# Performance work log

Hardware: AMD Instinct MI355X
Metric: run time of the kernel (lower is better)

## Reference

```python
import jax, jax.numpy as jnp
import numpy as np

PATCH = 128
FEATHER = 4  # config.fusion_feather_size
EPS = 1e-8


def _gaussian2d(f):
    k = 2 * f + 1
    sigma = f / 3.0
    x = jnp.arange(k, dtype=jnp.float32) - f
    g = jnp.exp(-0.5 * (x / sigma) ** 2)
    g = g / g.sum()
    return g[:, None] * g[None, :]


def setup_inputs() -> dict:
    key = jax.random.key(0)
    k1, k2, k3, k4, k5 = jax.random.split(key, 5)
    H, W, N = 2160, 3840, 256
    original_image = jax.random.normal(k1, (1, 3, H, W), jnp.float32)
    repaired_patches = jax.random.normal(k2, (N, 3, PATCH, PATCH), jnp.float32)
    holes_mask = (jax.random.uniform(k3, (1, 1, H, W)) < 0.05).astype(jnp.float32)
    pos_y = jax.random.randint(k4, (N,), 0, H - PATCH, jnp.int32)
    pos_x = jax.random.randint(k5, (N,), 0, W - PATCH, jnp.int32)
    return {"original_image": original_image, "repaired_patches": repaired_patches,
            "holes_mask": holes_mask, "pos_y": pos_y, "pos_x": pos_x}


def _feather_masks(holes_mask, pos_y, pos_x):
    # gather per-patch hole regions [N,P,P] (positions are constants -> parallel gather)
    m = holes_mask[0, 0]
    gather = jax.vmap(lambda y, x: jax.lax.dynamic_slice(m, (y, x), (PATCH, PATCH)))
    holes = gather(pos_y, pos_x)  # [N,P,P]
    kern = _gaussian2d(FEATHER)[None, None]  # [1,1,9,9]
    fm = jax.lax.conv_general_dilated(
        holes[:, None], kern, (1, 1), [(FEATHER, FEATHER), (FEATHER, FEATHER)])
    return fm[:, 0]  # [N,P,P]


def _masked_stats(img, nh):
    # per-channel masked mean/std over H,W (nh broadcasts over channels)
    denom = jnp.sum(nh, axis=(2, 3), keepdims=True)
    mean = jnp.sum(img * nh, axis=(2, 3), keepdims=True) / denom
    std = jnp.sqrt(jnp.sum((img - mean) ** 2 * nh, axis=(2, 3), keepdims=True) / denom)
    return mean, std


def reference(original_image, repaired_patches, holes_mask, pos_y, pos_x):
    fm = _feather_masks(holes_mask, pos_y, pos_x)  # [N,P,P]
    result0 = original_image[0]  # [3,H,W]

    # sequential scatter: each patch blends against the current result (patches may overlap)
    def step(res, inp):
        patch, f, y, x = inp
        region = jax.lax.dynamic_slice(res, (0, y, x), (3, PATCH, PATCH))
        fused = region * (1.0 - f[None]) + patch * f[None]
        return jax.lax.dynamic_update_slice(res, fused, (0, y, x)), None

    result, _ = jax.lax.scan(step, result0, (repaired_patches, fm, pos_y, pos_x))
    fused_image = result[None]  # [1,3,H,W]

    # color correction: match hole-region stats to original non-hole stats
    nh = 1.0 - holes_mask
    om, os = _masked_stats(original_image, nh)
    fmn, fs = _masked_stats(fused_image, nh)
    hole_region = fused_image * holes_mask
    corrected_hole = (hole_region - fmn) * (os / (fs + EPS)) + om
    corrected = fused_image * (1.0 - holes_mask) + corrected_hole * holes_mask
    return corrected
```

## Files before the change

kernel.cpp:

```cpp
#include <hip/hip_runtime.h>

#define HH 2160
#define WW 3840
#define NPATCH 256
#define PSZ 128
#define HW_ (HH*WW)
#define FMSZ (NPATCH*PSZ*PSZ)

#define TW 256
#define TH 8
#define NBX (WW/TW)
#define NBY (HH/TH)
#define NB  (NBX*NBY)
#define TSTRIDE (NPATCH+1)

typedef float fx4 __attribute__((ext_vector_type(4)));
typedef float fx4u __attribute__((ext_vector_type(4), aligned(4)));
typedef unsigned char uchar;

#define COEF_OFF  ((size_t)FMSZ*4)
#define PART_OFF  (COEF_OFF + 64)
#define HBB_OFF   ((PART_OFF + (size_t)13*NB*4 + 63)/64*64)
#define TLIST_OFF ((HBB_OFF + (size_t)(HW_/4) + 63)/64*64)
#define WS_NEED   (TLIST_OFF + (size_t)NB*TSTRIDE*4)

#define BARLDS() do { \
    asm volatile("s_waitcnt lgkmcnt(0)" ::: "memory"); \
    __builtin_amdgcn_s_barrier(); \
    asm volatile("" ::: "memory"); \
} while (0)

__global__ __launch_bounds__(256) void hbb_kernel(
        const float* __restrict__ mask, uchar* __restrict__ hbb) {
    const int q = blockIdx.x * 256 + threadIdx.x;
    if (q >= (HW_ >> 2)) return;
    const fx4 m = ((const fx4*)mask)[q];
    hbb[q] = (uchar)((unsigned)(m.x!=0.f) | ((unsigned)(m.y!=0.f)<<1)
                   | ((unsigned)(m.z!=0.f)<<2) | ((unsigned)(m.w!=0.f)<<3));
}

__global__ __launch_bounds__(256) void tlist_kernel(
        const int* __restrict__ pos_y, const int* __restrict__ pos_x,
        unsigned int* __restrict__ tlist) {
    __shared__ unsigned long long wm[4];
    const int tile = blockIdx.x;
    const int tx0 = (tile % NBX) * TW;
    const int ty0 = (tile / NBX) * TH;
    const int tid = threadIdx.x;
    const int lane = tid & 63;
    const int wid  = tid >> 6;
    const int yn = pos_y[tid], xn = pos_x[tid];
    const bool cov = (yn < ty0 + TH) && (yn + PSZ > ty0) &&
                     (xn < tx0 + TW) && (xn + PSZ > tx0);
    unsigned long long b = __ballot(cov);
    if (lane == 0) wm[wid] = b;
    __syncthreads();
    unsigned int* tl = tlist + (size_t)tile * TSTRIDE;
    if (cov) {
        int pos = __popcll(b & ((1ull << lane) - 1ull));
        for (int w = 0; w < wid; ++w) pos += __popcll(wm[w]);
        tl[1 + pos] = ((unsigned)tid << 24) | ((unsigned)yn << 12) | (unsigned)xn;
    }
    if (tid == 0)
        tl[0] = (unsigned)(__popcll(wm[0]) + __popcll(wm[1]) + __popcll(wm[2]) + __popcll(wm[3]));
}

__global__ __launch_bounds__(256) void feather_kernel(
        const float* __restrict__ mask, const uchar* __restrict__ hbb,
        const int* __restrict__ pos_y, const int* __restrict__ pos_x,
        float* __restrict__ fm) {
    __shared__ float sm[40*PSZ];
    __shared__ float tp[40*PSZ];
    const int n = blockIdx.x;
    const int r0 = blockIdx.y * 32;
    const int y0 = pos_y[n], x0 = pos_x[n];
    float g[9]; float s = 0.f;
    #pragma unroll
    for (int k = 0; k < 9; ++k) { float xx = (k-4)*0.75f; g[k] = expf(-0.5f*xx*xx); s += g[k]; }
    const float inv = 1.f/s;
    #pragma unroll
    for (int k = 0; k < 9; ++k) g[k] *= inv;

    for (int idx = threadIdx.x; idx < 40*PSZ; idx += 256) {
        int l = idx >> 7, j = idx & 127;
        int r = r0 + l - 4;
        float mv = 0.f;
        if ((unsigned)r < (unsigned)PSZ) {
            const int pix = (y0+r)*WW + (x0+j);
            if (hbb) mv = (float)((hbb[pix >> 2] >> (pix & 3)) & 1u);
            else     mv = mask[pix];
        }
        sm[idx] = mv;
    }
    __syncthreads();
    for (int idx = threadIdx.x; idx < 40*PSZ; idx += 256) {
        int l = idx >> 7, j = idx & 127;
        float a = 0.f;
        #pragma unroll
        for (int d = -4; d <= 4; ++d) {
            int jj = j + d;
            if (jj >= 0 && jj < PSZ) a += sm[(l<<7)+jj]*g[d+4];
        }
        tp[idx] = a;
    }
    __syncthreads();
    float* o = fm + n*(PSZ*PSZ) + r0*PSZ;
    for (int idx = threadIdx.x; idx < 32*PSZ; idx += 256) {
        int i = idx >> 7, j = idx & 127;
        float a = 0.f;
        #pragma unroll
        for (int d = 0; d < 9; ++d) a += tp[((i+d)<<7)+j]*g[d];
        o[idx] = a;
    }
}

__global__ __launch_bounds__(512) void compose_kernel(
        const float* __restrict__ orig, const float* __restrict__ patches,
        const float* __restrict__ fm, float* __restrict__ out,
        float* __restrict__ partial, const uchar* __restrict__ hbb,
        const unsigned int* __restrict__ tlist) {
    __shared__ float sv[5][520];

    const int tid = threadIdx.x;
    const int lane = tid & 63;
    const int wid  = tid >> 6;
    const int tx0 = blockIdx.x * TW;
    const int ty0 = blockIdx.y * TH;
    const int chan = blockIdx.z;

    const int x0 = tx0 + lane * 4;
    const int y  = ty0 + wid;
    const int q = (y*WW + x0) >> 2;
    const int pq = chan*(HW_ >> 2) + q;

    const fx4* __restrict__ orig4 = (const fx4*)orig;
    fx4* __restrict__ out4 = (fx4*)out;

    const uchar hbv = hbb[q];
    fx4 v = __builtin_nontemporal_load(&orig4[pq]);

    const unsigned int* __restrict__ tl =
        tlist + (size_t)(blockIdx.y * NBX + blockIdx.x) * TSTRIDE;
    const int cnt = (int)tl[0];

    const float nhx = (hbv & 1u) ? 0.f : 1.f;
    const float nhy = (hbv & 2u) ? 0.f : 1.f;
    const float nhz = (hbv & 4u) ? 0.f : 1.f;
    const float nhw = (hbv & 8u) ? 0.f : 1.f;

    const float a_cnt = nhx+nhy+nhz+nhw;
    const float s1o = v.x*nhx+v.y*nhy+v.z*nhz+v.w*nhw;
    const float s2o = v.x*v.x*nhx+v.y*v.y*nhy+v.z*v.z*nhz+v.w*v.w*nhw;

    for (int k = 0; k < cnt; ++k) {
        const unsigned e = tl[1 + k];
        const int xk = (int)(e & 0xFFFu);
        const int yk = (int)((e >> 12) & 0xFFFu);
        const int nn = (int)(e >> 24);
        const int dy = y - yk;
        if ((unsigned)dy >= (unsigned)PSZ) continue;
        const int dx0 = x0 - xk;
        if (dx0 <= -4 || dx0 >= PSZ) continue;
        const int rowb = dy << 7;
        const float* __restrict__ fmp = fm + nn*(PSZ*PSZ) + rowb;
        const float* __restrict__ pp  = patches + (nn*3 + chan)*(PSZ*PSZ) + rowb;
        if ((unsigned)dx0 <= (unsigned)(PSZ-4)) {
            const fx4u f4 = *(const fx4u*)(fmp + dx0);
            const fx4u p4 = *(const fx4u*)(pp + dx0);
            v.x += f4.x * (p4.x - v.x);
            v.y += f4.y * (p4.y - v.y);
            v.z += f4.z * (p4.z - v.z);
            v.w += f4.w * (p4.w - v.w);
        } else {
            #define BLEND(J, MX) { \
                const int dx = dx0 + J; \
                if ((unsigned)dx < (unsigned)PSZ) { \
                    const float f = fmp[dx]; \
                    v.MX += f * (pp[dx] - v.MX); \
                } }
            BLEND(0, x) BLEND(1, y) BLEND(2, z) BLEND(3, w)
            #undef BLEND
        }
    }

    out4[pq] = v;

    const float s1f = v.x*nhx+v.y*nhy+v.z*nhz+v.w*nhw;
    const float s2f = v.x*v.x*nhx+v.y*v.y*nhy+v.z*v.z*nhz+v.w*v.w*nhw;

    sv[0][tid] = s1o; sv[1][tid] = s2o; sv[2][tid] = s1f; sv[3][tid] = s2f; sv[4][tid] = a_cnt;
    BARLDS();
    if (wid < 5 && !(wid == 4 && chan != 0)) {
        const float* p = sv[wid];
        float t = p[lane] + p[lane+64] + p[lane+128] + p[lane+192]
                + p[lane+256] + p[lane+320] + p[lane+384] + p[lane+448];
        t += __shfl_down(t, 32); t += __shfl_down(t, 16);
        t += __shfl_down(t, 8);  t += __shfl_down(t, 4);
        t += __shfl_down(t, 2);  t += __shfl_down(t, 1);
        if (lane == 0) {
            const int bid = blockIdx.y * NBX + blockIdx.x;
            const int stat = (wid == 4) ? 0 : (1 + 3*wid + chan);
            partial[stat*NB + bid] = t;
        }
    }
}

__global__ __launch_bounds__(512) void compose_fb_kernel(
        const float* __restrict__ orig, const float* __restrict__ patches,
        const float* __restrict__ mask, const int* __restrict__ pos_y,
        const int* __restrict__ pos_x, const float* __restrict__ fm,
        float* __restrict__ out, float* __restrict__ partial) {
    __shared__ int ln[NPATCH];
    __shared__ int ly[NPATCH];
    __shared__ int lx[NPATCH];
    __shared__ unsigned long long wm[4];
    __shared__ float sv[5][520];

    const int tid = threadIdx.x;
    const int lane = tid & 63;
    const int wid  = tid >> 6;
    const int tx0 = blockIdx.x * TW;
    const int ty0 = blockIdx.y * TH;
    const int chan = blockIdx.z;

    const int x0 = tx0 + lane * 4;
    const int y  = ty0 + wid;
    const int q = (y*WW + x0) >> 2;
    const int pq = chan*(HW_ >> 2) + q;

    const fx4* __restrict__ orig4 = (const fx4*)orig;
    fx4* __restrict__ out4 = (fx4*)out;

    const fx4 mq = ((const fx4*)mask)[q];
    fx4 v = __builtin_nontemporal_load(&orig4[pq]);

    if (tid < NPATCH) {
        const int yn = pos_y[tid], xn = pos_x[tid];
        const bool cov = (yn < ty0 + TH) && (yn + PSZ > ty0) &&
                         (xn < tx0 + TW) && (xn + PSZ > tx0);
        unsigned long long b = __ballot(cov);
        if (lane == 0) wm[wid] = b;
        BARLDS();
        if (cov) {
            int pos = __popcll(b & ((1ull << lane) - 1ull));
            for (int w = 0; w < wid; ++w) pos += __popcll(wm[w]);
            ln[pos] = tid; ly[pos] = yn; lx[pos] = xn;
        }
    } else {
        BARLDS();
    }
    BARLDS();
    const int cnt = __popcll(wm[0]) + __popcll(wm[1]) + __popcll(wm[2]) + __popcll(wm[3]);

    const float nhx = 1.f-mq.x, nhy = 1.f-mq.y, nhz = 1.f-mq.z, nhw = 1.f-mq.w;
    const float a_cnt = nhx+nhy+nhz+nhw;
    const float s1o = v.x*nhx+v.y*nhy+v.z*nhz+v.w*nhw;
    const float s2o = v.x*v.x*nhx+v.y*v.y*nhy+v.z*v.z*nhz+v.w*v.w*nhw;

    for (int k = 0; k < cnt; ++k) {
        const int dy = y - ly[k];
        if ((unsigned)dy >= (unsigned)PSZ) continue;
        const int dx0 = x0 - lx[k];
        if (dx0 <= -4 || dx0 >= PSZ) continue;
        const int nn = ln[k];
        const int rowb = dy << 7;
        const float* __restrict__ fmp = fm + nn*(PSZ*PSZ) + rowb;
        const float* __restrict__ pp  = patches + (nn*3 + chan)*(PSZ*PSZ) + rowb;
        if ((unsigned)dx0 <= (unsigned)(PSZ-4)) {
            const fx4u f4 = *(const fx4u*)(fmp + dx0);
            const fx4u p4 = *(const fx4u*)(pp + dx0);
            v.x += f4.x * (p4.x - v.x);
            v.y += f4.y * (p4.y - v.y);
            v.z += f4.z * (p4.z - v.z);
            v.w += f4.w * (p4.w - v.w);
        } else {
            #define BLEND(J, MX) { \
                const int dx = dx0 + J; \
                if ((unsigned)dx < (unsigned)PSZ) { \
                    const float f = fmp[dx]; \
                    v.MX += f * (pp[dx] - v.MX); \
                } }
            BLEND(0, x) BLEND(1, y) BLEND(2, z) BLEND(3, w)
            #undef BLEND
        }
    }

    out4[pq] = v;

    const float s1f = v.x*nhx+v.y*nhy+v.z*nhz+v.w*nhw;
    const float s2f = v.x*v.x*nhx+v.y*v.y*nhy+v.z*v.z*nhz+v.w*v.w*nhw;

    sv[0][tid] = s1o; sv[1][tid] = s2o; sv[2][tid] = s1f; sv[3][tid] = s2f; sv[4][tid] = a_cnt;
    BARLDS();
    if (wid < 5 && !(wid == 4 && chan != 0)) {
        const float* p = sv[wid];
        float t = p[lane] + p[lane+64] + p[lane+128] + p[lane+192]
                + p[lane+256] + p[lane+320] + p[lane+384] + p[lane+448];
        t += __shfl_down(t, 32); t += __shfl_down(t, 16);
        t += __shfl_down(t, 8);  t += __shfl_down(t, 4);
        t += __shfl_down(t, 2);  t += __shfl_down(t, 1);
        if (lane == 0) {
            const int bid = blockIdx.y * NBX + blockIdx.x;
            const int stat = (wid == 4) ? 0 : (1 + 3*wid + chan);
            partial[stat*NB + bid] = t;
        }
    }
}

__global__ __launch_bounds__(832) void finalize_kernel(
        const float* __restrict__ partial, float* __restrict__ coef) {
    __shared__ double tot[13];
    const int w = threadIdx.x >> 6;
    const int lane = threadIdx.x & 63;
    const float* p = partial + w*NB;
    double s0 = 0.0, s1 = 0.0;
    int b = lane;
    for (; b + 64 < NB; b += 128) { s0 += (double)p[b]; s1 += (double)p[b+64]; }
    if (b < NB) s0 += (double)p[b];
    double t = s0 + s1;
    t += __shfl_down(t, 32); t += __shfl_down(t, 16);
    t += __shfl_down(t, 8);  t += __shfl_down(t, 4);
    t += __shfl_down(t, 2);  t += __shfl_down(t, 1);
    if (lane == 0) tot[w] = t;
    __syncthreads();
    if (threadIdx.x == 0) {
        const double cnt = tot[0];
        for (int c = 0; c < 3; ++c) {
            double om = tot[1+c]/cnt;
            double ov = tot[4+c]/cnt - om*om;
            double os = sqrt(ov > 0.0 ? ov : 0.0);
            double fmn = tot[7+c]/cnt;
            double fv = tot[10+c]/cnt - fmn*fmn;
            double fs = sqrt(fv > 0.0 ? fv : 0.0);
            coef[c]   = (float)(os/(fs + 1e-8));
            coef[3+c] = (float)fmn;
            coef[6+c] = (float)om;
        }
    }
}

__global__ __launch_bounds__(256) void correct_kernel(
        float* __restrict__ out, const uchar* __restrict__ hbb,
        const float* __restrict__ coef) {
    const int q = blockIdx.x * 256 + threadIdx.x;
    if (q >= (HW_ >> 2)) return;
    const unsigned bits = hbb[q];
    if (!bits) return;
    const float r0 = coef[0], r1 = coef[1], r2 = coef[2];
    const float f0 = coef[3], f1 = coef[4], f2 = coef[5];
    const float o0 = coef[6], o1 = coef[7], o2 = coef[8];
    fx4* __restrict__ out4 = (fx4*)out;
    fx4 v0 = out4[q];
    fx4 v1 = out4[(HW_>>2)+q];
    fx4 v2 = out4[((2*HW_)>>2)+q];
    if (bits & 1u) { v0.x=(v0.x-f0)*r0+o0; v1.x=(v1.x-f1)*r1+o1; v2.x=(v2.x-f2)*r2+o2; }
    if (bits & 2u) { v0.y=(v0.y-f0)*r0+o0; v1.y=(v1.y-f1)*r1+o1; v2.y=(v2.y-f2)*r2+o2; }
    if (bits & 4u) { v0.z=(v0.z-f0)*r0+o0; v1.z=(v1.z-f1)*r1+o1; v2.z=(v2.z-f2)*r2+o2; }
    if (bits & 8u) { v0.w=(v0.w-f0)*r0+o0; v1.w=(v1.w-f1)*r1+o1; v2.w=(v2.w-f2)*r2+o2; }
    out4[q] = v0;
    out4[(HW_>>2)+q] = v1;
    out4[((2*HW_)>>2)+q] = v2;
}

__global__ __launch_bounds__(256) void correct_full_kernel(
        float* __restrict__ out, const float* __restrict__ mask,
        const float* __restrict__ coef) {
    const int q = blockIdx.x * 256 + threadIdx.x;
    if (q >= (HW_ >> 2)) return;
    const fx4 m = ((const fx4*)mask)[q];
    if (m.x == 0.f && m.y == 0.f && m.z == 0.f && m.w == 0.f) return;
    const float r0 = coef[0], r1 = coef[1], r2 = coef[2];
    const float f0 = coef[3], f1 = coef[4], f2 = coef[5];
    const float o0 = coef[6], o1 = coef[7], o2 = coef[8];
    fx4* __restrict__ out4 = (fx4*)out;
    fx4 v0 = out4[q];
    fx4 v1 = out4[(HW_>>2)+q];
    fx4 v2 = out4[((2*HW_)>>2)+q];
    if (m.x != 0.f) { v0.x=(v0.x-f0)*r0+o0; v1.x=(v1.x-f1)*r1+o1; v2.x=(v2.x-f2)*r2+o2; }
    if (m.y != 0.f) { v0.y=(v0.y-f0)*r0+o0; v1.y=(v1.y-f1)*r1+o1; v2.y=(v2.y-f2)*r2+o2; }
    if (m.z != 0.f) { v0.z=(v0.z-f0)*r0+o0; v1.z=(v1.z-f1)*r1+o1; v2.z=(v2.z-f2)*r2+o2; }
    if (m.w != 0.f) { v0.w=(v0.w-f0)*r0+o0; v1.w=(v1.w-f1)*r1+o1; v2.w=(v2.w-f2)*r2+o2; }
    out4[q] = v0;
    out4[(HW_>>2)+q] = v1;
    out4[((2*HW_)>>2)+q] = v2;
}

extern "C" void kernel_launch(void* const* d_in, const int* in_sizes, int n_in,
                              void* d_out, int out_size, void* d_ws, size_t ws_size,
                              hipStream_t stream) {
    const float* orig    = (const float*)d_in[0];
    const float* patches = (const float*)d_in[1];
    const float* mask    = (const float*)d_in[2];
    const int*   pos_y   = (const int*)d_in[3];
    const int*   pos_x   = (const int*)d_in[4];
    float* out = (float*)d_out;

    float*        fm      = (float*)d_ws;
    float*        coef    = (float*)((char*)d_ws + COEF_OFF);
    float*        partial = (float*)((char*)d_ws + PART_OFF);
    uchar*        hbb     = (uchar*)((char*)d_ws + HBB_OFF);
    unsigned int* tlist   = (unsigned int*)((char*)d_ws + TLIST_OFF);

    const bool fast = (ws_size >= WS_NEED);

    dim3 fg(NPATCH, 4);
    dim3 g(NBX, NBY, 3);
    if (fast) {
        hbb_kernel<<<((HW_ >> 2) + 255)/256, 256, 0, stream>>>(mask, hbb);
        tlist_kernel<<<NB, 256, 0, stream>>>(pos_y, pos_x, tlist);
        feather_kernel<<<fg, 256, 0, stream>>>(mask, hbb, pos_y, pos_x, fm);
        compose_kernel<<<g, 512, 0, stream>>>(orig, patches, fm, out, partial, hbb, tlist);
        finalize_kernel<<<1, 832, 0, stream>>>(partial, coef);
        correct_kernel<<<((HW_ >> 2) + 255)/256, 256, 0, stream>>>(out, hbb, coef);
    } else {
        feather_kernel<<<fg, 256, 0, stream>>>(mask, nullptr, pos_y, pos_x, fm);
        compose_fb_kernel<<<g, 512, 0, stream>>>(orig, patches, mask, pos_y, pos_x, fm,
                                                 out, partial);
        finalize_kernel<<<1, 832, 0, stream>>>(partial, coef);
        correct_full_kernel<<<((HW_ >> 2) + 255)/256, 256, 0, stream>>>(out, mask, coef);
    }
}
```

Baseline: 128.4 us.

## Shrink compose blocks, per-row wave reductions, fuse hbb+tlist, split finalize

Merges the hole-bitmap and tile-list kernels into one launch. Compose blocks shrink from 512 to 128 threads, two rows per block. Each wave reduces its own stats with shuffles and writes per-row partials, so the LDS buffer and barrier are gone. The single-block finalize becomes a 13-block parallel reduction plus a tiny coefficient kernel. The aim is fewer barriers and a less serialized tail, at the cost of more blocks, more partial writes and one extra launch.

```diff
diff --git a/kernel.cpp b/kernel.cpp
--- a/kernel.cpp
+++ b/kernel.cpp
@@ -12,15 +12,17 @@
 #define NBX (WW/TW)
 #define NBY (HH/TH)
 #define NB  (NBX*NBY)
+#define NROW (NBX*HH)
 #define TSTRIDE (NPATCH+1)
 
 typedef float fx4 __attribute__((ext_vector_type(4)));
 typedef float fx4u __attribute__((ext_vector_type(4), aligned(4)));
 typedef unsigned char uchar;
 
-#define COEF_OFF  ((size_t)FMSZ*4)
-#define PART_OFF  (COEF_OFF + 64)
-#define HBB_OFF   ((PART_OFF + (size_t)13*NB*4 + 63)/64*64)
+#define TOT_OFF   ((size_t)FMSZ*4)
+#define COEF_OFF  (TOT_OFF + 104)
+#define PART_OFF  (TOT_OFF + 192)
+#define HBB_OFF   ((PART_OFF + (size_t)13*NROW*4 + 63)/64*64)
 #define TLIST_OFF ((HBB_OFF + (size_t)(HW_/4) + 63)/64*64)
 #define WS_NEED   (TLIST_OFF + (size_t)NB*TSTRIDE*4)
 
@@ -30,17 +32,9 @@
     asm volatile("" ::: "memory"); \
 } while (0)
 
-__global__ __launch_bounds__(256) void hbb_kernel(
-        const float* __restrict__ mask, uchar* __restrict__ hbb) {
-    const int q = blockIdx.x * 256 + threadIdx.x;
-    if (q >= (HW_ >> 2)) return;
-    const fx4 m = ((const fx4*)mask)[q];
-    hbb[q] = (uchar)((unsigned)(m.x!=0.f) | ((unsigned)(m.y!=0.f)<<1)
-                   | ((unsigned)(m.z!=0.f)<<2) | ((unsigned)(m.w!=0.f)<<3));
-}
-
-__global__ __launch_bounds__(256) void tlist_kernel(
-        const int* __restrict__ pos_y, const int* __restrict__ pos_x,
+__global__ __launch_bounds__(256) void hbbtl_kernel(
+        const float* __restrict__ mask, const int* __restrict__ pos_y,
+        const int* __restrict__ pos_x, uchar* __restrict__ hbb,
         unsigned int* __restrict__ tlist) {
     __shared__ unsigned long long wm[4];
     const int tile = blockIdx.x;
@@ -49,6 +43,17 @@
     const int tid = threadIdx.x;
     const int lane = tid & 63;
     const int wid  = tid >> 6;
+
+    #pragma unroll
+    for (int h = 0; h < 2; ++h) {
+        const int l = tid + h*256;
+        const int row = l >> 6, col = l & 63;
+        const int q = (ty0+row)*(WW >> 2) + (tx0 >> 2) + col;
+        const fx4 m = ((const fx4*)mask)[q];
+        hbb[q] = (uchar)((unsigned)(m.x!=0.f) | ((unsigned)(m.y!=0.f)<<1)
+                       | ((unsigned)(m.z!=0.f)<<2) | ((unsigned)(m.w!=0.f)<<3));
+    }
+
     const int yn = pos_y[tid], xn = pos_x[tid];
     const bool cov = (yn < ty0 + TH) && (yn + PSZ > ty0) &&
                      (xn < tx0 + TW) && (xn + PSZ > tx0);
@@ -114,22 +119,20 @@
     }
 }
 
-__global__ __launch_bounds__(512) void compose_kernel(
+__global__ __launch_bounds__(128) void compose_kernel(
         const float* __restrict__ orig, const float* __restrict__ patches,
         const float* __restrict__ fm, float* __restrict__ out,
         float* __restrict__ partial, const uchar* __restrict__ hbb,
         const unsigned int* __restrict__ tlist) {
-    __shared__ float sv[5][520];
-
     const int tid = threadIdx.x;
     const int lane = tid & 63;
-    const int wid  = tid >> 6;
-    const int tx0 = blockIdx.x * TW;
-    const int ty0 = blockIdx.y * TH;
+    const int w    = tid >> 6;
+    const int bx   = blockIdx.x;
+    const int y    = blockIdx.y * 2 + w;
     const int chan = blockIdx.z;
+    const int tx0  = bx * TW;
 
     const int x0 = tx0 + lane * 4;
-    const int y  = ty0 + wid;
     const int q = (y*WW + x0) >> 2;
     const int pq = chan*(HW_ >> 2) + q;
 
@@ -140,7 +143,7 @@
     fx4 v = __builtin_nontemporal_load(&orig4[pq]);
 
     const unsigned int* __restrict__ tl =
-        tlist + (size_t)(blockIdx.y * NBX + blockIdx.x) * TSTRIDE;
+        tlist + (size_t)((y >> 3) * NBX + bx) * TSTRIDE;
     const int cnt = (int)tl[0];
 
     const float nhx = (hbv & 1u) ? 0.f : 1.f;
@@ -188,21 +191,82 @@
     const float s1f = v.x*nhx+v.y*nhy+v.z*nhz+v.w*nhw;
     const float s2f = v.x*v.x*nhx+v.y*v.y*nhy+v.z*v.z*nhz+v.w*v.w*nhw;
 
-    sv[0][tid] = s1o; sv[1][tid] = s2o; sv[2][tid] = s1f; sv[3][tid] = s2f; sv[4][tid] = a_cnt;
-    BARLDS();
-    if (wid < 5 && !(wid == 4 && chan != 0)) {
-        const float* p = sv[wid];
-        float t = p[lane] + p[lane+64] + p[lane+128] + p[lane+192]
-                + p[lane+256] + p[lane+320] + p[lane+384] + p[lane+448];
+    float vals[5] = {s1o, s2o, s1f, s2f, a_cnt};
+    #pragma unroll
+    for (int i = 0; i < 5; ++i) {
+        float t = vals[i];
         t += __shfl_down(t, 32); t += __shfl_down(t, 16);
         t += __shfl_down(t, 8);  t += __shfl_down(t, 4);
         t += __shfl_down(t, 2);  t += __shfl_down(t, 1);
-        if (lane == 0) {
-            const int bid = blockIdx.y * NBX + blockIdx.x;
-            const int stat = (wid == 4) ? 0 : (1 + 3*wid + chan);
-            partial[stat*NB + bid] = t;
-        }
-    }
+        vals[i] = t;
+    }
+    if (lane == 0) {
+        const int rid = y * NBX + bx;
+        partial[(1+chan)*NROW  + rid] = vals[0];
+        partial[(4+chan)*NROW  + rid] = vals[1];
+        partial[(7+chan)*NROW  + rid] = vals[2];
+        partial[(10+chan)*NROW + rid] = vals[3];
+        if (chan == 0) partial[rid] = vals[4];
+    }
+}
+
+__global__ __launch_bounds__(256) void finalize1_kernel(
+        const float* __restrict__ partial, double* __restrict__ tot) {
+    __shared__ double red[4];
+    const int s = blockIdx.x;
+    const int tid = threadIdx.x;
+    const int lane = tid & 63;
+    const int wid  = tid >> 6;
+    const float* p = partial + (size_t)s*NROW;
+    double acc = 0.0;
+    for (int i = tid; i < NROW; i += 256) acc += (double)p[i];
+    acc += __shfl_down(acc, 32); acc += __shfl_down(acc, 16);
+    acc += __shfl_down(acc, 8);  acc += __shfl_down(acc, 4);
+    acc += __shfl_down(acc, 2);  acc += __shfl_down(acc, 1);
+    if (lane == 0) red[wid] = acc;
+    __syncthreads();
+    if (tid == 0) tot[s] = red[0] + red[1] + red[2] + red[3];
+}
+
+__global__ __launch_bounds__(64) void coef_kernel(
+        const double* __restrict__ tot, float* __restrict__ coef) {
+    if (threadIdx.x == 0) {
+        const double cnt = tot[0];
+        for (int c = 0; c < 3; ++c) {
+            double om = tot[1+c]/cnt;
+            double ov = tot[4+c]/cnt - om*om;
+            double os = sqrt(ov > 0.0 ? ov : 0.0);
+            double fmn = tot[7+c]/cnt;
+            double fv = tot[10+c]/cnt - fmn*fmn;
+            double fs = sqrt(fv > 0.0 ? fv : 0.0);
+            coef[c]   = (float)(os/(fs + 1e-8));
+            coef[3+c] = (float)fmn;
+            coef[6+c] = (float)om;
+        }
+    }
+}
+
+__global__ __launch_bounds__(256) void correct_kernel(
+        float* __restrict__ out, const uchar* __restrict__ hbb,
+        const float* __restrict__ coef) {
+    const int q = blockIdx.x * 256 + threadIdx.x;
+    if (q >= (HW_ >> 2)) return;
+    const unsigned bits = hbb[q];
+    if (!bits) return;
+    const float r0 = coef[0], r1 = coef[1], r2 = coef[2];
+    const float f0 = coef[3], f1 = coef[4], f2 = coef[5];
+    const float o0 = coef[6], o1 = coef[7], o2 = coef[8];
+    fx4* __restrict__ out4 = (fx4*)out;
+    fx4 v0 = out4[q];
+    fx4 v1 = out4[(HW_>>2)+q];
+    fx4 v2 = out4[((2*HW_)>>2)+q];
+    if (bits & 1u) { v0.x=(v0.x-f0)*r0+o0; v1.x=(v1.x-f1)*r1+o1; v2.x=(v2.x-f2)*r2+o2; }
+    if (bits & 2u) { v0.y=(v0.y-f0)*r0+o0; v1.y=(v1.y-f1)*r1+o1; v2.y=(v2.y-f2)*r2+o2; }
+    if (bits & 4u) { v0.z=(v0.z-f0)*r0+o0; v1.z=(v1.z-f1)*r1+o1; v2.z=(v2.z-f2)*r2+o2; }
+    if (bits & 8u) { v0.w=(v0.w-f0)*r0+o0; v1.w=(v1.w-f1)*r1+o1; v2.w=(v2.w-f2)*r2+o2; }
+    out4[q] = v0;
+    out4[(HW_>>2)+q] = v1;
+    out4[((2*HW_)>>2)+q] = v2;
 }
 
 __global__ __launch_bounds__(512) void compose_fb_kernel(
@@ -307,7 +371,7 @@
     }
 }
 
-__global__ __launch_bounds__(832) void finalize_kernel(
+__global__ __launch_bounds__(832) void finalize_fb_kernel(
         const float* __restrict__ partial, float* __restrict__ coef) {
     __shared__ double tot[13];
     const int w = threadIdx.x >> 6;
@@ -339,29 +403,6 @@
     }
 }
 
-__global__ __launch_bounds__(256) void correct_kernel(
-        float* __restrict__ out, const uchar* __restrict__ hbb,
-        const float* __restrict__ coef) {
-    const int q = blockIdx.x * 256 + threadIdx.x;
-    if (q >= (HW_ >> 2)) return;
-    const unsigned bits = hbb[q];
-    if (!bits) return;
-    const float r0 = coef[0], r1 = coef[1], r2 = coef[2];
-    const float f0 = coef[3], f1 = coef[4], f2 = coef[5];
-    const float o0 = coef[6], o1 = coef[7], o2 = coef[8];
-    fx4* __restrict__ out4 = (fx4*)out;
-    fx4 v0 = out4[q];
-    fx4 v1 = out4[(HW_>>2)+q];
-    fx4 v2 = out4[((2*HW_)>>2)+q];
-    if (bits & 1u) { v0.x=(v0.x-f0)*r0+o0; v1.x=(v1.x-f1)*r1+o1; v2.x=(v2.x-f2)*r2+o2; }
-    if (bits & 2u) { v0.y=(v0.y-f0)*r0+o0; v1.y=(v1.y-f1)*r1+o1; v2.y=(v2.y-f2)*r2+o2; }
-    if (bits & 4u) { v0.z=(v0.z-f0)*r0+o0; v1.z=(v1.z-f1)*r1+o1; v2.z=(v2.z-f2)*r2+o2; }
-    if (bits & 8u) { v0.w=(v0.w-f0)*r0+o0; v1.w=(v1.w-f1)*r1+o1; v2.w=(v2.w-f2)*r2+o2; }
-    out4[q] = v0;
-    out4[(HW_>>2)+q] = v1;
-    out4[((2*HW_)>>2)+q] = v2;
-}
-
 __global__ __launch_bounds__(256) void correct_full_kernel(
         float* __restrict__ out, const float* __restrict__ mask,
         const float* __restrict__ coef) {
@@ -396,6 +437,7 @@
     float* out = (float*)d_out;
 
     float*        fm      = (float*)d_ws;
+    double*       tot     = (double*)((char*)d_ws + TOT_OFF);
     float*        coef    = (float*)((char*)d_ws + COEF_OFF);
     float*        partial = (float*)((char*)d_ws + PART_OFF);
     uchar*        hbb     = (uchar*)((char*)d_ws + HBB_OFF);
@@ -404,19 +446,20 @@
     const bool fast = (ws_size >= WS_NEED);
 
     dim3 fg(NPATCH, 4);
-    dim3 g(NBX, NBY, 3);
     if (fast) {
-        hbb_kernel<<<((HW_ >> 2) + 255)/256, 256, 0, stream>>>(mask, hbb);
-        tlist_kernel<<<NB, 256, 0, stream>>>(pos_y, pos_x, tlist);
+        hbbtl_kernel<<<NB, 256, 0, stream>>>(mask, pos_y, pos_x, hbb, tlist);
         feather_kernel<<<fg, 256, 0, stream>>>(mask, hbb, pos_y, pos_x, fm);
-        compose_kernel<<<g, 512, 0, stream>>>(orig, patches, fm, out, partial, hbb, tlist);
-        finalize_kernel<<<1, 832, 0, stream>>>(partial, coef);
+        dim3 g(NBX, HH/2, 3);
+        compose_kernel<<<g, 128, 0, stream>>>(orig, patches, fm, out, partial, hbb, tlist);
+        finalize1_kernel<<<13, 256, 0, stream>>>(partial, tot);
+        coef_kernel<<<1, 64, 0, stream>>>(tot, coef);
         correct_kernel<<<((HW_ >> 2) + 255)/256, 256, 0, stream>>>(out, hbb, coef);
     } else {
+        dim3 g(NBX, NBY, 3);
         feather_kernel<<<fg, 256, 0, stream>>>(mask, nullptr, pos_y, pos_x, fm);
         compose_fb_kernel<<<g, 512, 0, stream>>>(orig, patches, mask, pos_y, pos_x, fm,
                                                  out, partial);
-        finalize_kernel<<<1, 832, 0, stream>>>(partial, coef);
+        finalize_fb_kernel<<<1, 832, 0, stream>>>(partial, coef);
         correct_full_kernel<<<((HW_ >> 2) + 255)/256, 256, 0, stream>>>(out, mask, coef);
     }
 }
```

New measurement: 158.8 us. +23.7%, slower.
